# Optimization experiments

Measured on AMD Instinct MI355X. Metric: run time of the kernel, lower is better.

Reference implementation:

```python
import jax, jax.numpy as jnp
import numpy as np

N = 50000      # nodes
E = 800000     # edges (avg degree 16)
F_IN = 128     # num_node_features
H = 128        # hidden_dim
G = 500        # num graphs in batch


def setup_inputs() -> dict:
    key = jax.random.key(0)
    ks = jax.random.split(key, 20)
    inp = {
        "x": jax.random.normal(ks[0], (N, F_IN), dtype=jnp.float32),
        "edge_index": jax.random.randint(ks[1], (2, E), 0, N, dtype=jnp.int32),
        "batch": jnp.sort(jax.random.randint(ks[2], (N,), 0, G, dtype=jnp.int32)),
    }
    s = 0.05
    # 3 GIN layers: MLP = Linear -> ReLU -> Linear, plus learnable eps (init 0)
    dims = [(F_IN, H), (H, H), (H, H)]
    for i, (din, dout) in enumerate(dims):
        k = jax.random.split(ks[3 + i], 4)
        inp[f"W1_{i}"] = jax.random.normal(k[0], (din, H), dtype=jnp.float32) * s
        inp[f"b1_{i}"] = jnp.zeros((H,), dtype=jnp.float32)
        inp[f"W2_{i}"] = jax.random.normal(k[1], (H, dout), dtype=jnp.float32) * s
        inp[f"b2_{i}"] = jnp.zeros((dout,), dtype=jnp.float32)
        inp[f"eps_{i}"] = jnp.zeros((), dtype=jnp.float32)
    inp["fc_w"] = jax.random.normal(ks[10], (H, 1), dtype=jnp.float32) * s
    inp["fc_b"] = jnp.zeros((1,), dtype=jnp.float32)
    return inp


def _gin_layer(x, src, dst, eps, W1, b1, W2, b2):
    # neighbor sum: scatter-add messages x[src] into dst rows
    agg = jax.ops.segment_sum(x[src], dst, num_segments=N)  # [N, d]
    h = (1.0 + eps) * x + agg
    h = jax.nn.relu(h @ W1 + b1) @ W2 + b2
    return h


def reference(x, edge_index, batch,
              W1_0, b1_0, W2_0, b2_0, eps_0,
              W1_1, b1_1, W2_1, b2_1, eps_1,
              W1_2, b1_2, W2_2, b2_2, eps_2,
              fc_w, fc_b):
    src, dst = edge_index[0], edge_index[1]
    layers = [(eps_0, W1_0, b1_0, W2_0, b2_0),
              (eps_1, W1_1, b1_1, W2_1, b2_1),
              (eps_2, W1_2, b1_2, W2_2, b2_2)]
    h = x
    for i, (eps, W1, b1, W2, b2) in enumerate(layers):
        h = _gin_layer(h, src, dst, eps, W1, b1, W2, b2)
        if i < len(layers) - 1:
            h = jax.nn.relu(h)  # dropout is identity in eval mode
    # global mean pool over graph ids
    sums = jax.ops.segment_sum(h, batch, num_segments=G)          # [G, H]
    counts = jax.ops.segment_sum(jnp.ones((N,), h.dtype), batch, num_segments=G)
    pooled = sums / jnp.maximum(counts, 1.0)[:, None]
    out = pooled @ fc_w + fc_b  # [G, 1]
    return jnp.squeeze(out, axis=-1)  # [G]
```

## Files before the change

### kernel.cpp

```cpp
#include <hip/hip_runtime.h>


#define FEAT 128
#define BCAP 2048
#define CHUNK 10240

typedef short  bf16x8 __attribute__((ext_vector_type(8)));
typedef float  f32x4  __attribute__((ext_vector_type(4)));

__device__ inline unsigned short f2bf(float f) {
    unsigned int u = __float_as_uint(f);
    u = (u + 0x7FFFu + ((u >> 16) & 1u)) >> 16;
    return (unsigned short)u;
}
__device__ inline float2 bfpair(unsigned int u) {
    float2 r;
    r.x = __uint_as_float(u << 16);
    r.y = __uint_as_float(u & 0xffff0000u);
    return r;
}

__global__ __launch_bounds__(1024) void bucket_kernel(
    const int* __restrict__ src, const int* __restrict__ dst,
    int* __restrict__ bcnt, unsigned int* __restrict__ bpairs, int E) {
    __shared__ unsigned int lpairs[CHUNK];
    __shared__ int lbase[1025];
    __shared__ int lcur[1024];
    __shared__ int lres[1024];
    __shared__ int part[1024];
    int tid = threadIdx.x;
    int e0 = blockIdx.x * CHUNK;
    int e1 = e0 + CHUNK; if (e1 > E) e1 = E;
    int cnt = e1 - e0;
    lcur[tid] = 0;
    __syncthreads();
    for (int e = e0 + tid; e < e1; e += 1024) atomicAdd(&lcur[dst[e] >> 6], 1);
    __syncthreads();
    int v = lcur[tid];
    part[tid] = v;
    __syncthreads();
    for (int d = 1; d < 1024; d <<= 1) {
        int u = (tid >= d) ? part[tid - d] : 0;
        __syncthreads();
        part[tid] += u;
        __syncthreads();
    }
    int ex = part[tid] - v;
    lbase[tid] = ex;
    if (tid == 1023) lbase[1024] = part[1023];
    lcur[tid] = ex;
    lres[tid] = (v > 0) ? atomicAdd(&bcnt[tid * 16], v) : 0;
    __syncthreads();
    for (int e = e0 + tid; e < e1; e += 1024) {
        int d = dst[e], s = src[e];
        int p = atomicAdd(&lcur[d >> 6], 1);
        lpairs[p] = ((unsigned int)s << 6) | (unsigned int)(d & 63);
    }
    __syncthreads();
    for (int j = tid; j < cnt; j += 1024) {
        int lo = 0, hi = 1023;
        while (lo < hi) { int m = (lo + hi + 1) >> 1; if (lbase[m] <= j) lo = m; else hi = m - 1; }
        int gpos = lres[lo] + (j - lbase[lo]);
        if (gpos < BCAP) bpairs[(size_t)lo * BCAP + gpos] = lpairs[j];
    }
}

__global__ __launch_bounds__(256) void deg_kernel(const int* __restrict__ bcnt,
                                                  const unsigned int* __restrict__ bpairs,
                                                  int* __restrict__ off, int n) {
    __shared__ int lh[64];
    int b = blockIdx.x, tid = threadIdx.x;
    if (tid < 64) lh[tid] = 0;
    __syncthreads();
    int cnt = bcnt[b * 16]; if (cnt > BCAP) cnt = BCAP;
    const unsigned int* bp = bpairs + (size_t)b * BCAP;
    for (int i = tid; i < cnt; i += 256) atomicAdd(&lh[bp[i] & 63u], 1);
    __syncthreads();
    if (tid < 64) {
        int node = b * 64 + tid;
        if (node < n) off[node] = lh[tid];
    }
}

__global__ void block_sum_kernel(const int* __restrict__ off, int* __restrict__ bs, int n) {
    int b = blockIdx.x, t = threadIdx.x;
    int base = b * 1024;
    int s = 0;
    #pragma unroll
    for (int i = 0; i < 4; ++i) {
        int idx = base + t + 256 * i;
        if (idx < n) s += off[idx];
    }
    #pragma unroll
    for (int d = 32; d; d >>= 1) s += __shfl_down(s, d, 64);
    __shared__ int ws[4];
    if ((t & 63) == 0) ws[t >> 6] = s;
    __syncthreads();
    if (t == 0) bs[b] = ws[0] + ws[1] + ws[2] + ws[3];
}

__global__ void scan_blocksums_kernel(int* __restrict__ bs, int nb,
                                      int* __restrict__ off, int n) {
    __shared__ int l[1024];
    int t = threadIdx.x;
    int v = (t < nb) ? bs[t] : 0;
    l[t] = v;
    __syncthreads();
    for (int d = 1; d < 1024; d <<= 1) {
        int u = (t >= d) ? l[t - d] : 0;
        __syncthreads();
        l[t] += u;
        __syncthreads();
    }
    if (t < nb) bs[t] = (t == 0) ? 0 : l[t - 1];
    if (t == 1023) off[n] = l[1023];
}

__global__ __launch_bounds__(256) void block_scan_kernel(
    int* __restrict__ off, const int* __restrict__ bs, int n) {
    __shared__ int l[1024];
    __shared__ int part[256];
    int b = blockIdx.x, t = threadIdx.x;
    int base = b * 1024;
    #pragma unroll
    for (int i = 0; i < 4; ++i) {
        int idx = base + t + 256 * i;
        l[t + 256 * i] = (idx < n) ? off[idx] : 0;
    }
    __syncthreads();
    int v0 = l[4 * t], v1 = l[4 * t + 1], v2 = l[4 * t + 2], v3 = l[4 * t + 3];
    int p = v0 + v1 + v2 + v3;
    part[t] = p;
    __syncthreads();
    for (int d = 1; d < 256; d <<= 1) {
        int u = (t >= d) ? part[t - d] : 0;
        __syncthreads();
        part[t] += u;
        __syncthreads();
    }
    int ex = bs[b] + ((t == 0) ? 0 : part[t - 1]);
    int e0 = ex, e1 = ex + v0, e2 = e1 + v1, e3 = e2 + v2;
    int idx = base + 4 * t;
    if (idx + 3 < n) {
        ((int4*)(off + idx))[0] = make_int4(e0, e1, e2, e3);
    } else {
        if (idx + 0 < n) off[idx + 0] = e0;
        if (idx + 1 < n) off[idx + 1] = e1;
        if (idx + 2 < n) off[idx + 2] = e2;
    }
}

__global__ __launch_bounds__(256) void bucket_scatter_kernel(
    const int* __restrict__ bcnt, const unsigned int* __restrict__ bpairs,
    const int* __restrict__ off, int* __restrict__ srcs, int n) {
    __shared__ int lcur[64];
    int b = blockIdx.x, tid = threadIdx.x;
    if (tid < 64) {
        int node = b * 64 + tid;
        lcur[tid] = (node < n) ? off[node] : 0;
    }
    __syncthreads();
    int cnt = bcnt[b * 16]; if (cnt > BCAP) cnt = BCAP;
    const unsigned int* bp = bpairs + (size_t)b * BCAP;
    for (int i = tid; i < cnt; i += 256) {
        unsigned int pr = bp[i];
        int pos = atomicAdd(&lcur[pr & 63u], 1);
        srcs[pos] = (int)(pr >> 6);
    }
}

__global__ __launch_bounds__(256) void setup_kernel(
    const float* __restrict__ x, unsigned int* __restrict__ xbf, long pairs, int nxb,
    const int* __restrict__ batch, int* __restrict__ gstart, int n, int G,
    const float* __restrict__ W2f, const float* __restrict__ b2f,
    const float* __restrict__ fcw, float* __restrict__ weff,
    const float* __restrict__ W0, const float* __restrict__ W1,
    const float* __restrict__ W2, const float* __restrict__ W3,
    const float* __restrict__ W4, unsigned short* __restrict__ Wswz) {
    int b = blockIdx.x, tid = threadIdx.x;
    if (b < nxb) {
        long i = (long)b * 256 + tid;
        if (i < pairs) {
            float2 v = ((const float2*)x)[i];
            unsigned int pk = (unsigned int)f2bf(v.x) | ((unsigned int)f2bf(v.y) << 16);
            long node = i >> 6;
            int dg = (int)(i & 63);
            int slice = dg >> 4, d = dg & 15;
            xbf[(size_t)slice * n * 16 + node * 16 + d] = pk;
        }
    } else if (b < nxb + 2) {
        int i = (b - nxb) * 256 + tid;
        if (i <= G) {
            int lo = 0, hi = n;
            while (lo < hi) { int m = (lo + hi) >> 1; if (batch[m] < i) lo = m + 1; else hi = m; }
            gstart[i] = lo;
        }
    } else if (b == nxb + 2) {
        int lane = tid & 63, wave = tid >> 6;
        float2 f2 = ((const float2*)fcw)[lane];
        for (int r = wave; r < 128; r += 4) {
            float2 w = ((const float2*)(W2f + r * FEAT))[lane];
            float d = w.x * f2.x + w.y * f2.y;
            #pragma unroll
            for (int s = 32; s; s >>= 1) d += __shfl_down(d, s, 64);
            if (lane == 0) weff[r] = d;
        }
        if (wave == 0) {
            float2 bb = ((const float2*)b2f)[lane];
            float d = bb.x * f2.x + bb.y * f2.y;
            #pragma unroll
            for (int s = 32; s; s >>= 1) d += __shfl_down(d, s, 64);
            if (lane == 0) weff[128] = d;
        }
    } else {
        int gid = (b - nxb - 3) * 256 + tid;
        if (gid < 5 * 2048) {
            int mat = gid >> 11;
            int task = gid & 2047;
            int c = task >> 4, m = task & 15;
            const float* W = (mat == 0) ? W0 : (mat == 1) ? W1 : (mat == 2) ? W2 :
                             (mat == 3) ? W3 : W4;
            unsigned short* dp = Wswz + mat * 16384 + c * 128 + ((m ^ (c & 7)) << 3);
            #pragma unroll
            for (int j = 0; j < 8; ++j) dp[j] = f2bf(W[(8 * m + j) * FEAT + c]);
        }
    }
}

__global__ __launch_bounds__(256) void agg_kernel(
    const unsigned int* __restrict__ hs, const int* __restrict__ off,
    const int* __restrict__ srcs, const float* __restrict__ eps_p,
    unsigned int* __restrict__ pre, int n) {
    int b = blockIdx.x;
    int slice = b & 3;
    int chunk = b >> 2;
    int tid = threadIdx.x;
    int wave = tid >> 6, lane = tid & 63;
    int g = lane >> 3, d = lane & 7;
    int node = chunk * 32 + wave * 8 + g;
    if (node >= n) return;
    float eps1 = 1.0f + eps_p[0];
    const uint2* hb = (const uint2*)(hs + (size_t)slice * n * 16);
    uint2 su = hb[(size_t)node * 8 + d];
    float2 sa = bfpair(su.x), sb = bfpair(su.y);
    float4 acc0 = make_float4(sa.x * eps1, sa.y * eps1, sb.x * eps1, sb.y * eps1);
    float4 acc1 = make_float4(0.f, 0.f, 0.f, 0.f);
    float4 acc2 = make_float4(0.f, 0.f, 0.f, 0.f);
    float4 acc3 = make_float4(0.f, 0.f, 0.f, 0.f);
    int j0 = off[node], j1 = off[node + 1];
    int j = j0;
    #define ACC(A, U) { float2 p0 = bfpair(U.x), p1 = bfpair(U.y); \
        A.x += p0.x; A.y += p0.y; A.z += p1.x; A.w += p1.y; }
    for (; j + 8 <= j1; j += 8) {
        int s0 = srcs[j], s1 = srcs[j + 1], s2 = srcs[j + 2], s3 = srcs[j + 3];
        int s4 = srcs[j + 4], s5 = srcs[j + 5], s6 = srcs[j + 6], s7 = srcs[j + 7];
        uint2 u0 = hb[(size_t)s0 * 8 + d];
        uint2 u1 = hb[(size_t)s1 * 8 + d];
        uint2 u2 = hb[(size_t)s2 * 8 + d];
        uint2 u3 = hb[(size_t)s3 * 8 + d];
        uint2 u4 = hb[(size_t)s4 * 8 + d];
        uint2 u5 = hb[(size_t)s5 * 8 + d];
        uint2 u6 = hb[(size_t)s6 * 8 + d];
        uint2 u7 = hb[(size_t)s7 * 8 + d];
        ACC(acc0, u0) ACC(acc1, u1) ACC(acc2, u2) ACC(acc3, u3)
        ACC(acc0, u4) ACC(acc1, u5) ACC(acc2, u6) ACC(acc3, u7)
    }
    for (; j + 4 <= j1; j += 4) {
        int s0 = srcs[j], s1 = srcs[j + 1], s2 = srcs[j + 2], s3 = srcs[j + 3];
        uint2 u0 = hb[(size_t)s0 * 8 + d];
        uint2 u1 = hb[(size_t)s1 * 8 + d];
        uint2 u2 = hb[(size_t)s2 * 8 + d];
        uint2 u3 = hb[(size_t)s3 * 8 + d];
        ACC(acc0, u0) ACC(acc1, u1) ACC(acc2, u2) ACC(acc3, u3)
    }
    for (; j < j1; ++j) {
        uint2 u = hb[(size_t)srcs[j] * 8 + d];
        ACC(acc0, u)
    }
    #undef ACC
    acc0.x += acc1.x + acc2.x;  acc0.y += acc1.y + acc2.y;
    acc0.z += acc1.z + acc2.z;  acc0.w += acc1.w + acc2.w;
    acc0.x += acc3.x;  acc0.y += acc3.y;
    acc0.z += acc3.z;  acc0.w += acc3.w;
    uint2 o;
    o.x = (unsigned int)f2bf(acc0.x) | ((unsigned int)f2bf(acc0.y) << 16);
    o.y = (unsigned int)f2bf(acc0.z) | ((unsigned int)f2bf(acc0.w) << 16);
    ((uint2*)(pre + (size_t)slice * n * 16))[(size_t)node * 8 + d] = o;
}

template <int MODE>
__global__ __launch_bounds__(256) void mfma_mlp_kernel(
    const unsigned short* __restrict__ A, const unsigned short* __restrict__ Wswz,
    const float* __restrict__ bias, unsigned short* __restrict__ outbf,
    const int* __restrict__ batch, const float* __restrict__ weff,
    float* __restrict__ sums, int n) {
    __shared__ int4 Wl4[2048];
    int tid = threadIdx.x;
    const int4* ws4 = (const int4*)Wswz;
    #pragma unroll
    for (int i = 0; i < 8; ++i) Wl4[i * 256 + tid] = ws4[i * 256 + tid];
    __syncthreads();
    const unsigned short* Wl = (const unsigned short*)Wl4;

    int lane = tid & 63, wave = tid >> 6;
    int q = lane >> 4, c15 = lane & 15;
    int r0 = blockIdx.x * 64 + wave * 16;
    int arow = r0 + c15;
    bool rv = arow < n;
    size_t sstride = (size_t)n * 32;
    const unsigned short* abase = A + (size_t)arow * 32 + 8 * q;

    f32x4 zf = {0.f, 0.f, 0.f, 0.f};
    f32x4 acc[8];
    #pragma unroll
    for (int i = 0; i < 8; ++i) acc[i] = zf;
    bf16x8 zero8 = {0, 0, 0, 0, 0, 0, 0, 0};

    #pragma unroll
    for (int k0 = 0; k0 < 4; ++k0) {
        bf16x8 a = rv ? *(const bf16x8*)(abase + (size_t)k0 * sstride) : zero8;
        int m = k0 * 4 + q;
        #pragma unroll
        for (int nt = 0; nt < 8; ++nt) {
            int col = nt * 16 + c15;
            bf16x8 bfr = *(const bf16x8*)&Wl[col * 128 + ((m ^ (col & 7)) << 3)];
            acc[nt] = __builtin_amdgcn_mfma_f32_16x16x32_bf16(a, bfr, acc[nt], 0, 0, 0);
        }
    }

    int orow0 = r0 + q * 4;
    if (MODE == 1) {
        #pragma unroll
        for (int nt = 0; nt < 8; ++nt) {
            float bv = bias[nt * 16 + c15];
            size_t sb = (size_t)(nt >> 1) * sstride + (nt & 1) * 16 + c15;
            #pragma unroll
            for (int r = 0; r < 4; ++r) {
                int ro = orow0 + r;
                if (ro < n) {
                    float v = fmaxf(acc[nt][r] + bv, 0.f);
                    outbf[sb + (size_t)ro * 32] = f2bf(v);
                }
            }
        }
    } else {
        __shared__ float gsum[64];
        int r0b = blockIdx.x * 64;
        int lastn = r0b + 63 < n - 1 ? r0b + 63 : n - 1;
        int gmin = batch[r0b];
        int gmax = batch[lastn];
        int span = gmax - gmin + 1;
        bool lds_ok = (span <= 64);
        if (lds_ok) for (int i = tid; i < span; i += 256) gsum[i] = 0.f;
        __syncthreads();
        float rowdot[4] = {0.f, 0.f, 0.f, 0.f};
        #pragma unroll
        for (int nt = 0; nt < 8; ++nt) {
            int col = nt * 16 + c15;
            float bv = bias[col];
            float wv = weff[col];
            #pragma unroll
            for (int r = 0; r < 4; ++r)
                rowdot[r] += fmaxf(acc[nt][r] + bv, 0.f) * wv;
        }
        #pragma unroll
        for (int r = 0; r < 4; ++r) {
            float v = rowdot[r];
            v += __shfl_xor(v, 1, 64);
            v += __shfl_xor(v, 2, 64);
            v += __shfl_xor(v, 4, 64);
            v += __shfl_xor(v, 8, 64);
            if (c15 == 0) {
                int node = orow0 + r;
                if (node < n) {
                    int g = batch[node];
                    if (lds_ok) atomicAdd(&gsum[g - gmin], v);
                    else        atomicAdd(&sums[g], v);
                }
            }
        }
        __syncthreads();
        if (lds_ok)
            for (int i = tid; i < span; i += 256) atomicAdd(&sums[gmin + i], gsum[i]);
    }
}

__global__ void finalize_kernel(const float* __restrict__ sums, const int* __restrict__ gstart,
                                const float* __restrict__ weff, const float* __restrict__ fcb,
                                float* __restrict__ out, int G) {
    int g = blockIdx.x * blockDim.x + threadIdx.x;
    if (g >= G) return;
    int cnt = gstart[g + 1] - gstart[g];
    out[g] = (cnt > 0) ? sums[g] / (float)cnt + weff[128] + fcb[0] : fcb[0];
}

static inline size_t align256(size_t x) { return (x + 255) & ~(size_t)255; }

extern "C" void kernel_launch(void* const* d_in, const int* in_sizes, int n_in,
                              void* d_out, int out_size, void* d_ws, size_t ws_size,
                              hipStream_t stream) {
    const float* x      = (const float*)d_in[0];
    const int*   ei     = (const int*)d_in[1];
    const int*   batch  = (const int*)d_in[2];
    const float* W1[3]  = {(const float*)d_in[3],  (const float*)d_in[8],  (const float*)d_in[13]};
    const float* b1[3]  = {(const float*)d_in[4],  (const float*)d_in[9],  (const float*)d_in[14]};
    const float* W2[3]  = {(const float*)d_in[5],  (const float*)d_in[10], (const float*)d_in[15]};
    const float* b2[3]  = {(const float*)d_in[6],  (const float*)d_in[11], (const float*)d_in[16]};
    const float* eps[3] = {(const float*)d_in[7],  (const float*)d_in[12], (const float*)d_in[17]};
    const float* fcw    = (const float*)d_in[18];
    const float* fcb    = (const float*)d_in[19];
    float* out = (float*)d_out;

    const int N = in_sizes[0] / FEAT;
    const int E = in_sizes[1] / 2;
    const int G = out_size;
    const int nbuckets = (N + 63) >> 6;

    char* p = (char*)d_ws;
    int* off    = (int*)p;  p += align256((size_t)(N + 1) * 4);
    int* srcs   = (int*)p;  p += align256((size_t)E * 4);
    int* bsums  = (int*)p;  p += align256((size_t)1024 * 4);
    int* gstart = (int*)p;  p += align256((size_t)(G + 1) * 4);
    float* weff = (float*)p; p += align256((size_t)256 * 4);
    unsigned short* Wswz = (unsigned short*)p; p += align256((size_t)5 * 16384 * 2);
    float* sums = (float*)p;
    char* z0 = (char*)sums;
    p += align256((size_t)G * 4);
    int* bcnt = (int*)p; p += align256((size_t)nbuckets * 16 * 4);
    size_t zbytes = (size_t)(p - z0);
    unsigned int* bpairs = (unsigned int*)p;     p += align256((size_t)nbuckets * BCAP * 4);
    unsigned int* x_bf   = (unsigned int*)p;     p += align256((size_t)N * 64 * 4);
    unsigned int* pre_bf = (unsigned int*)p;     p += align256((size_t)N * 64 * 4);
    unsigned int* t_bf   = (unsigned int*)p;     p += align256((size_t)N * 64 * 4);
    unsigned int* h_bf   = (unsigned int*)p;     p += align256((size_t)N * 64 * 4);
    (void)ws_size; (void)n_in;

    const int* src = ei;
    const int* dst = ei + E;

    hipMemsetAsync(z0, 0, zbytes, stream);

    const int nb = (N + 1023) / 1024;
    const int nchunks = (E + CHUNK - 1) / CHUNK;
    bucket_kernel<<<nchunks, 1024, 0, stream>>>(src, dst, bcnt, bpairs, E);
    deg_kernel<<<nbuckets, 256, 0, stream>>>(bcnt, bpairs, off, N);
    block_sum_kernel<<<nb, 256, 0, stream>>>(off, bsums, N);
    scan_blocksums_kernel<<<1, 1024, 0, stream>>>(bsums, nb, off, N);
    block_scan_kernel<<<nb, 256, 0, stream>>>(off, bsums, N);
    bucket_scatter_kernel<<<nbuckets, 256, 0, stream>>>(bcnt, bpairs, off, srcs, N);

    long pairs = (long)N * 64;
    int nxb = (int)((pairs + 255) / 256);
    setup_kernel<<<nxb + 43, 256, 0, stream>>>(
        x, x_bf, pairs, nxb, batch, gstart, N, G,
        W2[2], b2[2], fcw, weff,
        W1[0], W2[0], W1[1], W2[1], W1[2], Wswz);

    const int aggBlocks  = 4 * ((N + 31) / 32);
    const int gemmBlocks = (N + 63) / 64;
    const unsigned short* Wz[5] = {Wswz, Wswz + 16384, Wswz + 2 * 16384,
                                   Wswz + 3 * 16384, Wswz + 4 * 16384};

    const unsigned int* h = x_bf;
    for (int i = 0; i < 2; ++i) {
        agg_kernel<<<aggBlocks, 256, 0, stream>>>(h, off, srcs, eps[i], pre_bf, N);
        mfma_mlp_kernel<1><<<gemmBlocks, 256, 0, stream>>>(
            (const unsigned short*)pre_bf, Wz[2 * i], b1[i], (unsigned short*)t_bf,
            nullptr, nullptr, nullptr, N);
        mfma_mlp_kernel<1><<<gemmBlocks, 256, 0, stream>>>(
            (const unsigned short*)t_bf, Wz[2 * i + 1], b2[i], (unsigned short*)h_bf,
            nullptr, nullptr, nullptr, N);
        h = h_bf;
    }
    agg_kernel<<<aggBlocks, 256, 0, stream>>>(h, off, srcs, eps[2], pre_bf, N);
    mfma_mlp_kernel<2><<<gemmBlocks, 256, 0, stream>>>(
        (const unsigned short*)pre_bf, Wz[4], b1[2], nullptr,
        batch, weff, sums, N);

    finalize_kernel<<<(G + 255) / 256, 256, 0, stream>>>(sums, gstart, weff, fcb, out, G);
}
```

Baseline: 304.7 us.

## Fuse CSR build into bucket-count scan and widen aggregation loads to 16 bytes

Replaces the five-kernel degree/scan/scatter CSR construction with two kernels. A single-block scan over per-bucket counts is followed by one kernel per bucket that builds a local histogram, does an in-wave prefix scan, writes offsets and scatters sources. Separately, the aggregation kernel now gives each lane 16-byte loads covering 8 features, with 4 lanes per node, so each block handles twice as many nodes. This cuts launch count and global passes over the offsets, but raises register pressure in aggregation and relies on nbuckets fitting in 1024.

```diff
diff --git a/kernel.cpp b/kernel.cpp
--- a/kernel.cpp
+++ b/kernel.cpp
@@ -65,103 +65,51 @@
     }
 }
 
-__global__ __launch_bounds__(256) void deg_kernel(const int* __restrict__ bcnt,
-                                                  const unsigned int* __restrict__ bpairs,
-                                                  int* __restrict__ off, int n) {
+__global__ void scan_bcnt_kernel(const int* __restrict__ bcnt, int* __restrict__ bbase,
+                                 int* __restrict__ off, int n, int nbuckets) {
+    __shared__ int l[1024];
+    int t = threadIdx.x;
+    int v = (t < nbuckets) ? bcnt[t * 16] : 0;
+    l[t] = v;
+    __syncthreads();
+    for (int d = 1; d < 1024; d <<= 1) {
+        int u = (t >= d) ? l[t - d] : 0;
+        __syncthreads();
+        l[t] += u;
+        __syncthreads();
+    }
+    if (t < nbuckets) bbase[t] = l[t] - v;
+    if (t == 1023) off[n] = l[1023];
+}
+
+__global__ __launch_bounds__(256) void degscat_kernel(
+    const int* __restrict__ bcnt, const int* __restrict__ bbase,
+    const unsigned int* __restrict__ bpairs,
+    int* __restrict__ off, int* __restrict__ srcs, int n) {
     __shared__ int lh[64];
+    __shared__ int lcur[64];
     int b = blockIdx.x, tid = threadIdx.x;
     if (tid < 64) lh[tid] = 0;
     __syncthreads();
     int cnt = bcnt[b * 16]; if (cnt > BCAP) cnt = BCAP;
+    int base = bbase[b];
     const unsigned int* bp = bpairs + (size_t)b * BCAP;
     for (int i = tid; i < cnt; i += 256) atomicAdd(&lh[bp[i] & 63u], 1);
     __syncthreads();
     if (tid < 64) {
+        int v = lh[tid];
+        int inc = v;
+        #pragma unroll
+        for (int d = 1; d < 64; d <<= 1) {
+            int u = __shfl_up(inc, d, 64);
+            if (tid >= d) inc += u;
+        }
+        int ex = base + inc - v;
         int node = b * 64 + tid;
-        if (node < n) off[node] = lh[tid];
-    }
-}
-
-__global__ void block_sum_kernel(const int* __restrict__ off, int* __restrict__ bs, int n) {
-    int b = blockIdx.x, t = threadIdx.x;
-    int base = b * 1024;
-    int s = 0;
-    #pragma unroll
-    for (int i = 0; i < 4; ++i) {
-        int idx = base + t + 256 * i;
-        if (idx < n) s += off[idx];
-    }
-    #pragma unroll
-    for (int d = 32; d; d >>= 1) s += __shfl_down(s, d, 64);
-    __shared__ int ws[4];
-    if ((t & 63) == 0) ws[t >> 6] = s;
-    __syncthreads();
-    if (t == 0) bs[b] = ws[0] + ws[1] + ws[2] + ws[3];
-}
-
-__global__ void scan_blocksums_kernel(int* __restrict__ bs, int nb,
-                                      int* __restrict__ off, int n) {
-    __shared__ int l[1024];
-    int t = threadIdx.x;
-    int v = (t < nb) ? bs[t] : 0;
-    l[t] = v;
-    __syncthreads();
-    for (int d = 1; d < 1024; d <<= 1) {
-        int u = (t >= d) ? l[t - d] : 0;
-        __syncthreads();
-        l[t] += u;
-        __syncthreads();
-    }
-    if (t < nb) bs[t] = (t == 0) ? 0 : l[t - 1];
-    if (t == 1023) off[n] = l[1023];
-}
-
-__global__ __launch_bounds__(256) void block_scan_kernel(
-    int* __restrict__ off, const int* __restrict__ bs, int n) {
-    __shared__ int l[1024];
-    __shared__ int part[256];
-    int b = blockIdx.x, t = threadIdx.x;
-    int base = b * 1024;
-    #pragma unroll
-    for (int i = 0; i < 4; ++i) {
-        int idx = base + t + 256 * i;
-        l[t + 256 * i] = (idx < n) ? off[idx] : 0;
-    }
-    __syncthreads();
-    int v0 = l[4 * t], v1 = l[4 * t + 1], v2 = l[4 * t + 2], v3 = l[4 * t + 3];
-    int p = v0 + v1 + v2 + v3;
-    part[t] = p;
-    __syncthreads();
-    for (int d = 1; d < 256; d <<= 1) {
-        int u = (t >= d) ? part[t - d] : 0;
-        __syncthreads();
-        part[t] += u;
-        __syncthreads();
-    }
-    int ex = bs[b] + ((t == 0) ? 0 : part[t - 1]);
-    int e0 = ex, e1 = ex + v0, e2 = e1 + v1, e3 = e2 + v2;
-    int idx = base + 4 * t;
-    if (idx + 3 < n) {
-        ((int4*)(off + idx))[0] = make_int4(e0, e1, e2, e3);
-    } else {
-        if (idx + 0 < n) off[idx + 0] = e0;
-        if (idx + 1 < n) off[idx + 1] = e1;
-        if (idx + 2 < n) off[idx + 2] = e2;
-    }
-}
-
-__global__ __launch_bounds__(256) void bucket_scatter_kernel(
-    const int* __restrict__ bcnt, const unsigned int* __restrict__ bpairs,
-    const int* __restrict__ off, int* __restrict__ srcs, int n) {
-    __shared__ int lcur[64];
-    int b = blockIdx.x, tid = threadIdx.x;
-    if (tid < 64) {
-        int node = b * 64 + tid;
-        lcur[tid] = (node < n) ? off[node] : 0;
-    }
-    __syncthreads();
-    int cnt = bcnt[b * 16]; if (cnt > BCAP) cnt = BCAP;
-    const unsigned int* bp = bpairs + (size_t)b * BCAP;
+        if (node < n) off[node] = ex;
+        lcur[tid] = ex;
+    }
+    __syncthreads();
     for (int i = tid; i < cnt; i += 256) {
         unsigned int pr = bp[i];
         int pos = atomicAdd(&lcur[pr & 63u], 1);
@@ -236,56 +184,63 @@
     int chunk = b >> 2;
     int tid = threadIdx.x;
     int wave = tid >> 6, lane = tid & 63;
-    int g = lane >> 3, d = lane & 7;
-    int node = chunk * 32 + wave * 8 + g;
+    int g = lane >> 2, d = lane & 3;
+    int node = chunk * 64 + wave * 16 + g;
     if (node >= n) return;
     float eps1 = 1.0f + eps_p[0];
-    const uint2* hb = (const uint2*)(hs + (size_t)slice * n * 16);
-    uint2 su = hb[(size_t)node * 8 + d];
-    float2 sa = bfpair(su.x), sb = bfpair(su.y);
-    float4 acc0 = make_float4(sa.x * eps1, sa.y * eps1, sb.x * eps1, sb.y * eps1);
-    float4 acc1 = make_float4(0.f, 0.f, 0.f, 0.f);
-    float4 acc2 = make_float4(0.f, 0.f, 0.f, 0.f);
-    float4 acc3 = make_float4(0.f, 0.f, 0.f, 0.f);
+    const uint4* hb = (const uint4*)(hs + (size_t)slice * n * 16);
+    uint4 su = hb[(size_t)node * 4 + d];
+    float2 p0 = bfpair(su.x), p1 = bfpair(su.y), p2 = bfpair(su.z), p3 = bfpair(su.w);
+    float4 a0 = make_float4(p0.x * eps1, p0.y * eps1, p1.x * eps1, p1.y * eps1);
+    float4 b0 = make_float4(p2.x * eps1, p2.y * eps1, p3.x * eps1, p3.y * eps1);
+    float4 a1 = make_float4(0.f, 0.f, 0.f, 0.f), b1v = a1;
+    float4 a2 = a1, b2v = a1;
+    float4 a3 = a1, b3v = a1;
     int j0 = off[node], j1 = off[node + 1];
     int j = j0;
-    #define ACC(A, U) { float2 p0 = bfpair(U.x), p1 = bfpair(U.y); \
-        A.x += p0.x; A.y += p0.y; A.z += p1.x; A.w += p1.y; }
+    #define ACC(A, B, U) { float2 q0 = bfpair(U.x), q1 = bfpair(U.y), \
+                                  q2 = bfpair(U.z), q3 = bfpair(U.w); \
+        A.x += q0.x; A.y += q0.y; A.z += q1.x; A.w += q1.y; \
+        B.x += q2.x; B.y += q2.y; B.z += q3.x; B.w += q3.y; }
     for (; j + 8 <= j1; j += 8) {
         int s0 = srcs[j], s1 = srcs[j + 1], s2 = srcs[j + 2], s3 = srcs[j + 3];
         int s4 = srcs[j + 4], s5 = srcs[j + 5], s6 = srcs[j + 6], s7 = srcs[j + 7];
-        uint2 u0 = hb[(size_t)s0 * 8 + d];
-        uint2 u1 = hb[(size_t)s1 * 8 + d];
-        uint2 u2 = hb[(size_t)s2 * 8 + d];
-        uint2 u3 = hb[(size_t)s3 * 8 + d];
-        uint2 u4 = hb[(size_t)s4 * 8 + d];
-        uint2 u5 = hb[(size_t)s5 * 8 + d];
-        uint2 u6 = hb[(size_t)s6 * 8 + d];
-        uint2 u7 = hb[(size_t)s7 * 8 + d];
-        ACC(acc0, u0) ACC(acc1, u1) ACC(acc2, u2) ACC(acc3, u3)
-        ACC(acc0, u4) ACC(acc1, u5) ACC(acc2, u6) ACC(acc3, u7)
+        uint4 u0 = hb[(size_t)s0 * 4 + d];
+        uint4 u1 = hb[(size_t)s1 * 4 + d];
+        uint4 u2 = hb[(size_t)s2 * 4 + d];
+        uint4 u3 = hb[(size_t)s3 * 4 + d];
+        uint4 u4 = hb[(size_t)s4 * 4 + d];
+        uint4 u5 = hb[(size_t)s5 * 4 + d];
+        uint4 u6 = hb[(size_t)s6 * 4 + d];
+        uint4 u7 = hb[(size_t)s7 * 4 + d];
+        ACC(a0, b0, u0) ACC(a1, b1v, u1) ACC(a2, b2v, u2) ACC(a3, b3v, u3)
+        ACC(a0, b0, u4) ACC(a1, b1v, u5) ACC(a2, b2v, u6) ACC(a3, b3v, u7)
     }
     for (; j + 4 <= j1; j += 4) {
         int s0 = srcs[j], s1 = srcs[j + 1], s2 = srcs[j + 2], s3 = srcs[j + 3];
-        uint2 u0 = hb[(size_t)s0 * 8 + d];
-        uint2 u1 = hb[(size_t)s1 * 8 + d];
-        uint2 u2 = hb[(size_t)s2 * 8 + d];
-        uint2 u3 = hb[(size_t)s3 * 8 + d];
-        ACC(acc0, u0) ACC(acc1, u1) ACC(acc2, u2) ACC(acc3, u3)
+        uint4 u0 = hb[(size_t)s0 * 4 + d];
+        uint4 u1 = hb[(size_t)s1 * 4 + d];
+        uint4 u2 = hb[(size_t)s2 * 4 + d];
+        uint4 u3 = hb[(size_t)s3 * 4 + d];
+        ACC(a0, b0, u0) ACC(a1, b1v, u1) ACC(a2, b2v, u2) ACC(a3, b3v, u3)
     }
     for (; j < j1; ++j) {
-        uint2 u = hb[(size_t)srcs[j] * 8 + d];
-        ACC(acc0, u)
+        uint4 u = hb[(size_t)srcs[j] * 4 + d];
+        ACC(a0, b0, u)
     }
     #undef ACC
-    acc0.x += acc1.x + acc2.x;  acc0.y += acc1.y + acc2.y;
-    acc0.z += acc1.z + acc2.z;  acc0.w += acc1.w + acc2.w;
-    acc0.x += acc3.x;  acc0.y += acc3.y;
-    acc0.z += acc3.z;  acc0.w += acc3.w;
-    uint2 o;
-    o.x = (unsigned int)f2bf(acc0.x) | ((unsigned int)f2bf(acc0.y) << 16);
-    o.y = (unsigned int)f2bf(acc0.z) | ((unsigned int)f2bf(acc0.w) << 16);
-    ((uint2*)(pre + (size_t)slice * n * 16))[(size_t)node * 8 + d] = o;
+    a0.x += a1.x + a2.x;  a0.y += a1.y + a2.y;
+    a0.z += a1.z + a2.z;  a0.w += a1.w + a2.w;
+    a0.x += a3.x;  a0.y += a3.y;  a0.z += a3.z;  a0.w += a3.w;
+    b0.x += b1v.x + b2v.x;  b0.y += b1v.y + b2v.y;
+    b0.z += b1v.z + b2v.z;  b0.w += b1v.w + b2v.w;
+    b0.x += b3v.x;  b0.y += b3v.y;  b0.z += b3v.z;  b0.w += b3v.w;
+    uint4 o;
+    o.x = (unsigned int)f2bf(a0.x) | ((unsigned int)f2bf(a0.y) << 16);
+    o.y = (unsigned int)f2bf(a0.z) | ((unsigned int)f2bf(a0.w) << 16);
+    o.z = (unsigned int)f2bf(b0.x) | ((unsigned int)f2bf(b0.y) << 16);
+    o.w = (unsigned int)f2bf(b0.z) | ((unsigned int)f2bf(b0.w) << 16);
+    ((uint4*)(pre + (size_t)slice * n * 16))[(size_t)node * 4 + d] = o;
 }
 
 template <int MODE>
@@ -419,7 +374,7 @@
     char* p = (char*)d_ws;
     int* off    = (int*)p;  p += align256((size_t)(N + 1) * 4);
     int* srcs   = (int*)p;  p += align256((size_t)E * 4);
-    int* bsums  = (int*)p;  p += align256((size_t)1024 * 4);
+    int* bbase  = (int*)p;  p += align256((size_t)1024 * 4);
     int* gstart = (int*)p;  p += align256((size_t)(G + 1) * 4);
     float* weff = (float*)p; p += align256((size_t)256 * 4);
     unsigned short* Wswz = (unsigned short*)p; p += align256((size_t)5 * 16384 * 2);
@@ -440,14 +395,10 @@
 
     hipMemsetAsync(z0, 0, zbytes, stream);
 
-    const int nb = (N + 1023) / 1024;
     const int nchunks = (E + CHUNK - 1) / CHUNK;
     bucket_kernel<<<nchunks, 1024, 0, stream>>>(src, dst, bcnt, bpairs, E);
-    deg_kernel<<<nbuckets, 256, 0, stream>>>(bcnt, bpairs, off, N);
-    block_sum_kernel<<<nb, 256, 0, stream>>>(off, bsums, N);
-    scan_blocksums_kernel<<<1, 1024, 0, stream>>>(bsums, nb, off, N);
-    block_scan_kernel<<<nb, 256, 0, stream>>>(off, bsums, N);
-    bucket_scatter_kernel<<<nbuckets, 256, 0, stream>>>(bcnt, bpairs, off, srcs, N);
+    scan_bcnt_kernel<<<1, 1024, 0, stream>>>(bcnt, bbase, off, N, nbuckets);
+    degscat_kernel<<<nbuckets, 256, 0, stream>>>(bcnt, bbase, bpairs, off, srcs, N);
 
     long pairs = (long)N * 64;
     int nxb = (int)((pairs + 255) / 256);
@@ -456,7 +407,7 @@
         W2[2], b2[2], fcw, weff,
         W1[0], W2[0], W1[1], W2[1], W1[2], Wswz);
 
-    const int aggBlocks  = 4 * ((N + 31) / 32);
+    const int aggBlocks  = 4 * ((N + 63) / 64);
     const int gemmBlocks = (N + 63) / 64;
     const unsigned short* Wz[5] = {Wswz, Wswz + 16384, Wswz + 2 * 16384,
                                    Wswz + 3 * 16384, Wswz + 4 * 16384};
```

After: 295.5 us. 3.0% less time.
